# Performance work log

Measured on AMD Instinct MI355X. Metric: run time of the kernel, lower is better.

The kernel has to match this reference:

```python
import jax, jax.numpy as jnp
import numpy as np

D = 768
H = 12
DH = D // H
EPS = 1e-5

def _ln(x, g, b):
    m = jnp.mean(x, axis=-1, keepdims=True)
    v = jnp.mean(jnp.square(x - m), axis=-1, keepdims=True)
    return (x - m) * jax.lax.rsqrt(v + EPS) * g + b

def _gelu_new(x):
    c = jnp.float32(0.7978845608028654)  # sqrt(2/pi)
    return 0.5 * x * (1.0 + jnp.tanh(c * (x + 0.044715 * x * x * x)))

def setup_inputs() -> dict:
    key = jax.random.key(0)
    ks = jax.random.split(key, 12)
    s = lambda fan: 1.0 / np.sqrt(fan)
    return {
        "x": jax.random.normal(ks[0], (2, 1024, D), jnp.float32),
        "context_seq": jax.random.normal(ks[1], (2, 256, D), jnp.float32),
        "sos_h": jnp.zeros((D,), jnp.float32),
        "ln1_g": jnp.ones((D,), jnp.float32),
        "ln1_b": jnp.zeros((D,), jnp.float32),
        "W_attn": jax.random.normal(ks[2], (D, 3 * D), jnp.float32) * s(D),
        "b_attn": jnp.zeros((3 * D,), jnp.float32),
        "W_ref": jax.random.normal(ks[3], (D, 2 * D), jnp.float32) * s(D),
        "b_ref": jnp.zeros((2 * D,), jnp.float32),
        "W_proj": jax.random.normal(ks[4], (D, D), jnp.float32) * s(D),
        "b_proj": jnp.zeros((D,), jnp.float32),
        "ln2_g": jnp.ones((D,), jnp.float32),
        "ln2_b": jnp.zeros((D,), jnp.float32),
        "W_fc": jax.random.normal(ks[5], (D, 4 * D), jnp.float32) * s(D),
        "b_fc": jnp.zeros((4 * D,), jnp.float32),
        "W_mproj": jax.random.normal(ks[6], (4 * D, D), jnp.float32) * s(4 * D),
        "b_mproj": jnp.zeros((D,), jnp.float32),
    }

def _split_heads(t):  # [B,T,D] -> [B,H,T,dh]
    B, T, _ = t.shape
    return t.reshape(B, T, H, DH).transpose(0, 2, 1, 3)

def reference(x, context_seq, sos_h, ln1_g, ln1_b, W_attn, b_attn, W_ref, b_ref,
              W_proj, b_proj, ln2_g, ln2_b, W_fc, b_fc, W_mproj, b_mproj):
    B, S, _ = x.shape
    Sc = context_seq.shape[1]
    # prepend sos token (history_seq is None, history_seq_len = 0)
    sos = jnp.broadcast_to(sos_h.reshape(1, 1, D), (B, 1, D))
    h = jnp.concatenate([sos, x], axis=1)          # [B, S+1, D]
    hl = _ln(h, ln1_g, ln1_b)
    qkv = hl @ W_attn + b_attn
    q, k, v = jnp.split(qkv, 3, axis=-1)
    ckv = context_seq @ W_ref + b_ref
    kc, vc = jnp.split(ckv, 2, axis=-1)
    K = jnp.concatenate([kc, k], axis=1)            # [B, Sc+S+1, D]
    V = jnp.concatenate([vc, v], axis=1)
    qh, kh, vh = _split_heads(q), _split_heads(K), _split_heads(V)
    nd, ns = S + 1, Sc + S + 1
    w = jnp.einsum('bhqd,bhkd->bhqk', qh, kh) / jnp.float32(np.sqrt(DH))
    # causal bias window: query i attends to key j iff j <= i + Sc
    mask = jnp.arange(ns)[None, :] <= (jnp.arange(nd)[:, None] + Sc)
    w = jnp.where(mask[None, None], w, jnp.float32(-10000.0))
    w = jax.nn.softmax(w, axis=-1)
    a = jnp.einsum('bhqk,bhkd->bhqd', w, vh)        # [B,H,S+1,dh]
    a = a.transpose(0, 2, 1, 3).reshape(B, nd, D)
    a = a @ W_proj + b_proj
    h = h + a
    m = _gelu_new(_ln(h, ln2_g, ln2_b) @ W_fc + b_fc) @ W_mproj + b_mproj
    h = h + m
    return h[:, 1:, :]                               # drop sos position
```

## Files before the change

### kernel.cpp

```cpp
#include <hip/hip_runtime.h>
#include <math.h>

#define D0 768
#define NH 12
#define DHD 64
#define NB 2
#define SQ 1024
#define SCX 256
#define ND 1025
#define NS 1281
#define TT (NB*ND)
#define TP 2176
#define TC (NB*SCX)

typedef __attribute__((ext_vector_type(8))) short bf16x8;
typedef __attribute__((ext_vector_type(4))) float f32x4;

typedef const __attribute__((address_space(1))) unsigned int* gptr_t;
typedef __attribute__((address_space(3))) unsigned int* lptr_t;

__device__ __forceinline__ unsigned short f2bf(float f) {
    union { float f; unsigned u; } v; v.f = f;
    unsigned r = v.u + 0x7FFFu + ((v.u >> 16) & 1u);
    return (unsigned short)(r >> 16);
}

__device__ __forceinline__ float gelu_new(float x) {
    float x3 = x*x*x;
    float u = 0.7978845608028654f*(x + 0.044715f*x3);
    return 0.5f*x*(1.f + tanhf(u));
}

struct PrepArgs {
    const float* x; const float* sos; float* h;
    const float* ctx; unsigned short* ctxb;
    const float* W[5]; unsigned short* Wt[5];
    int K[5], N[5], nblk[5];
};

#define NBH 1538
#define NCVT 192

__global__ __launch_bounds__(256) void k_prep(PrepArgs a) {
    __shared__ float t[32][33];
    const int tid = threadIdx.x;
    int bid = blockIdx.x;
    if (bid < NBH) {
        int idx = bid*256 + tid;
        if (idx < TT*192) {
            int r = idx/192, c4 = idx%192;
            int b = r/ND, tt = r%ND;
            float4 v;
            if (tt == 0) v = ((const float4*)a.sos)[c4];
            else         v = ((const float4*)a.x)[(size_t)(b*SQ + tt - 1)*192 + c4];
            ((float4*)a.h)[(size_t)r*192 + c4] = v;
        }
        return;
    }
    bid -= NBH;
    if (bid < NCVT) {
        int i = bid*256 + tid;
        float4 p = ((const float4*)a.ctx)[i*2];
        float4 q = ((const float4*)a.ctx)[i*2+1];
        uint4 o;
        o.x = (unsigned)f2bf(p.x) | ((unsigned)f2bf(p.y) << 16);
        o.y = (unsigned)f2bf(p.z) | ((unsigned)f2bf(p.w) << 16);
        o.z = (unsigned)f2bf(q.x) | ((unsigned)f2bf(q.y) << 16);
        o.w = (unsigned)f2bf(q.z) | ((unsigned)f2bf(q.w) << 16);
        ((uint4*)a.ctxb)[i] = o;
        return;
    }
    bid -= NCVT;
    #pragma unroll
    for (int wi = 0; wi < 5; ++wi) {
        if (bid < a.nblk[wi]) {
            const float* W = a.W[wi];
            unsigned short* Wt = a.Wt[wi];
            const int K = a.K[wi], N = a.N[wi];
            const int nbx = N >> 5;
            const int n0 = (bid % nbx)*32, k0 = (bid / nbx)*32;
            const int r = tid >> 3, c4 = (tid & 7)*4;
            float4 v = *(const float4*)&W[(size_t)(k0+r)*N + n0 + c4];
            t[r][c4+0]=v.x; t[r][c4+1]=v.y; t[r][c4+2]=v.z; t[r][c4+3]=v.w;
            __syncthreads();
            ushort4 o;
            o.x = f2bf(t[c4+0][r]); o.y = f2bf(t[c4+1][r]);
            o.z = f2bf(t[c4+2][r]); o.w = f2bf(t[c4+3][r]);
            *(ushort4*)&Wt[(size_t)(n0+r)*K + k0 + c4] = o;
            return;
        }
        bid -= a.nblk[wi];
    }
}

__global__ __launch_bounds__(256) void k_ln(const float* __restrict__ in,
                                            const float* __restrict__ add,
                                            const float* __restrict__ g,
                                            const float* __restrict__ beta,
                                            unsigned short* __restrict__ out,
                                            float* __restrict__ resid,
                                            int nvalid) {
    int r = blockIdx.x;
    int tid = threadIdx.x;
    const size_t base = (size_t)r*D0;
    if (r >= nvalid) {
        out[base+tid] = 0; out[base+tid+256] = 0; out[base+tid+512] = 0;
        return;
    }
    float v0 = in[base+tid], v1 = in[base+tid+256], v2 = in[base+tid+512];
    if (add) {
        v0 += add[base+tid]; v1 += add[base+tid+256]; v2 += add[base+tid+512];
        resid[base+tid] = v0; resid[base+tid+256] = v1; resid[base+tid+512] = v2;
    }
    float s = v0+v1+v2;
    float ss = v0*v0 + v1*v1 + v2*v2;
    #pragma unroll
    for (int o = 32; o >= 1; o >>= 1) {
        s  += __shfl_down(s, o);
        ss += __shfl_down(ss, o);
    }
    __shared__ float red[8];
    __shared__ float mv[2];
    int w = tid >> 6;
    if ((tid & 63) == 0) { red[w] = s; red[4+w] = ss; }
    __syncthreads();
    if (tid == 0) {
        float S1 = red[0]+red[1]+red[2]+red[3];
        float S2 = red[4]+red[5]+red[6]+red[7];
        float mean = S1 * (1.f/D0);
        float var  = S2 * (1.f/D0) - mean*mean;
        mv[0] = mean; mv[1] = rsqrtf(var + 1e-5f);
    }
    __syncthreads();
    float mean = mv[0], rstd = mv[1];
    out[base+tid]     = f2bf((v0-mean)*rstd*g[tid]     + beta[tid]);
    out[base+tid+256] = f2bf((v1-mean)*rstd*g[tid+256] + beta[tid+256]);
    out[base+tid+512] = f2bf((v2-mean)*rstd*g[tid+512] + beta[tid+512]);
}

template<int GELU, int OUTBF>
__device__ __forceinline__ void gemm64_body(unsigned short* As, unsigned short* Bs,
                                            const unsigned short* __restrict__ A,
                                            const unsigned short* __restrict__ Bt,
                                            const float* __restrict__ bias,
                                            void* __restrict__ Cv,
                                            int N, int K, int bx, int by) {
    const int tid = threadIdx.x;
    const int w = tid >> 6;
    const int l = tid & 63;
    const int wm = w >> 1, wn = w & 1;
    const int m0 = by * 64, n0 = bx * 64;

    f32x4 acc[2][2] = {};

    for (int k0 = 0; k0 < K; k0 += 64) {
        __syncthreads();
        #pragma unroll
        for (int i = 0; i < 2; ++i) {
            int s = i*256 + tid;
            int row = s >> 3;
            int ch  = (s & 7) ^ (row & 7);
            const unsigned short* ga = A  + (size_t)(m0 + row)*K + k0 + ch*8;
            const unsigned short* gb = Bt + (size_t)(n0 + row)*K + k0 + ch*8;
            lptr_t la = (lptr_t)(As + (i*256 + w*64)*8);
            lptr_t lb = (lptr_t)(Bs + (i*256 + w*64)*8);
            __builtin_amdgcn_global_load_lds((gptr_t)ga, la, 16, 0, 0);
            __builtin_amdgcn_global_load_lds((gptr_t)gb, lb, 16, 0, 0);
        }
        __syncthreads();
        #pragma unroll
        for (int kc = 0; kc < 2; ++kc) {
            const int kchunk = kc*4 + (l >> 4);
            bf16x8 a[2], b[2];
            #pragma unroll
            for (int mi = 0; mi < 2; ++mi) {
                int row = wm*32 + mi*16 + (l & 15);
                a[mi] = *(const bf16x8*)&As[row*64 + ((kchunk ^ (row & 7))*8)];
            }
            #pragma unroll
            for (int ni = 0; ni < 2; ++ni) {
                int row = wn*32 + ni*16 + (l & 15);
                b[ni] = *(const bf16x8*)&Bs[row*64 + ((kchunk ^ (row & 7))*8)];
            }
            #pragma unroll
            for (int mi = 0; mi < 2; ++mi)
                #pragma unroll
                for (int ni = 0; ni < 2; ++ni)
                    acc[mi][ni] = __builtin_amdgcn_mfma_f32_16x16x32_bf16(a[mi], b[ni], acc[mi][ni], 0, 0, 0);
        }
    }

    float* Cf = (float*)Cv;
    unsigned short* Cb = (unsigned short*)Cv;
    const int rbase = m0 + wm*32 + (l >> 4)*4;
    const int cbase = n0 + wn*32 + (l & 15);
    #pragma unroll
    for (int ni = 0; ni < 2; ++ni) {
        int col = cbase + ni*16;
        float bv = bias[col];
        #pragma unroll
        for (int mi = 0; mi < 2; ++mi) {
            #pragma unroll
            for (int r = 0; r < 4; ++r) {
                int row = rbase + mi*16 + r;
                float v = acc[mi][ni][r] + bv;
                if (GELU) v = gelu_new(v);
                if (OUTBF) Cb[(size_t)row*N + col] = f2bf(v);
                else       Cf[(size_t)row*N + col] = v;
            }
        }
    }
}

template<int GELU, int OUTBF>
__global__ __launch_bounds__(256) void k_gemm64(const unsigned short* __restrict__ A,
                                                const unsigned short* __restrict__ Bt,
                                                const float* __restrict__ bias,
                                                void* __restrict__ Cv,
                                                int N, int K) {
    __shared__ unsigned short As[64*64];
    __shared__ unsigned short Bs[64*64];
    gemm64_body<GELU,OUTBF>(As, Bs, A, Bt, bias, Cv, N, K, blockIdx.x, blockIdx.y);
}

__global__ __launch_bounds__(256) void k_gemm_qkvckv(const unsigned short* __restrict__ hlb,
                                                     const unsigned short* __restrict__ WatT,
                                                     const float* __restrict__ bat,
                                                     unsigned short* __restrict__ qkvb,
                                                     const unsigned short* __restrict__ ctxb,
                                                     const unsigned short* __restrict__ WrefT,
                                                     const float* __restrict__ bref,
                                                     unsigned short* __restrict__ ckvb) {
    __shared__ unsigned short As[64*64];
    __shared__ unsigned short Bs[64*64];
    int bid = blockIdx.x;
    if (bid < (2304/64)*(TP/64)) {
        gemm64_body<0,1>(As, Bs, hlb, WatT, bat, qkvb, 2304, 768, bid % (2304/64), bid / (2304/64));
    } else {
        bid -= (2304/64)*(TP/64);
        gemm64_body<0,1>(As, Bs, ctxb, WrefT, bref, ckvb, 1536, 768, bid % (1536/64), bid / (1536/64));
    }
}

__global__ __launch_bounds__(256, 4) void k_attn_mfma(const unsigned short* __restrict__ qkvb,
                                                      const unsigned short* __restrict__ ckvb,
                                                      unsigned short* __restrict__ attnob) {
    const int bh = blockIdx.y;
    const int b = bh / NH, hh = bh % NH;
    const int tid = threadIdx.x;
    const int w = tid >> 6;
    const int l = tid & 63;
    const int lg = l >> 4;
    const int ll = l & 15;

    const int q0 = (64 - blockIdx.x) * 16;

    __shared__ unsigned short lds_u16[18432];
    unsigned short* Kw = lds_u16 + w*4608;
    unsigned short* Vw = Kw + 2048;
    unsigned short* Pw = Kw + 4096;

    bf16x8 qf[2];
    {
        int qc = min(q0 + ll, ND-1);
        const unsigned short* qrow = qkvb + (size_t)(b*ND + qc)*2304 + hh*64;
        qf[0] = *(const bf16x8*)(qrow + lg*8);
        qf[1] = *(const bf16x8*)(qrow + 32 + lg*8);
    }

    f32x4 o_acc[4] = {};
    float mrow[4], lrow[4];
    #pragma unroll
    for (int i = 0; i < 4; ++i) { mrow[i] = -1e30f; lrow[i] = 0.f; }

    const int klim = min(q0 + 15 + SCX, NS-1);

    for (int kt = w; kt*32 <= klim; kt += 4) {
        #pragma unroll
        for (int it = 0; it < 4; ++it) {
            int slot = it*64 + l;
            int key  = slot >> 3;
            int ch   = (slot & 7) ^ (key & 7);
            int kg   = min(kt*32 + key, NS-1);
            const unsigned short* src = (kg < SCX)
                ? ckvb + (size_t)(b*SCX + kg)*1536 + hh*64 + ch*8
                : qkvb + (size_t)(b*ND + kg - SCX)*2304 + 768 + hh*64 + ch*8;
            __builtin_amdgcn_global_load_lds((gptr_t)src, (lptr_t)(Kw + it*512), 16, 0, 0);
        }
        #pragma unroll
        for (int it = 0; it < 2; ++it) {
            int kp  = l & 15;
            int dch = (l >> 4) + it*4;
            int kv0 = kp*2;
            int kg0 = min(kt*32 + kv0,     NS-1);
            int kg1 = min(kt*32 + kv0 + 1, NS-1);
            const unsigned short* s0 = (kg0 < SCX)
                ? ckvb + (size_t)(b*SCX + kg0)*1536 + 768 + hh*64 + dch*8
                : qkvb + (size_t)(b*ND + kg0 - SCX)*2304 + 1536 + hh*64 + dch*8;
            const unsigned short* s1 = (kg1 < SCX)
                ? ckvb + (size_t)(b*SCX + kg1)*1536 + 768 + hh*64 + dch*8
                : qkvb + (size_t)(b*ND + kg1 - SCX)*2304 + 1536 + hh*64 + dch*8;
            union { uint4 u; unsigned short s[8]; } r0, r1;
            r0.u = *(const uint4*)s0;
            r1.u = *(const uint4*)s1;
            #pragma unroll
            for (int j = 0; j < 8; ++j) {
                int d = dch*8 + j;
                unsigned val = (unsigned)r0.s[j] | ((unsigned)r1.s[j] << 16);
                *(unsigned*)(Vw + d*32 + (((kp>>2) ^ ((d>>2)&3))*8) + (kp&3)*2) = val;
            }
        }
        asm volatile("s_waitcnt vmcnt(0) lgkmcnt(0)" ::: "memory");
        __builtin_amdgcn_sched_barrier(0);

        bf16x8 kf[2][2];
        #pragma unroll
        for (int c = 0; c < 2; ++c) {
            int key = c*16 + ll;
            #pragma unroll
            for (int kc = 0; kc < 2; ++kc)
                kf[c][kc] = *(const bf16x8*)(Kw + key*64 + (((kc*4 + lg) ^ (key&7))*8));
        }
        f32x4 s_acc[2];
        #pragma unroll
        for (int c = 0; c < 2; ++c) {
            f32x4 z = {0.f, 0.f, 0.f, 0.f};
            z = __builtin_amdgcn_mfma_f32_16x16x32_bf16(qf[0], kf[c][0], z, 0, 0, 0);
            s_acc[c] = __builtin_amdgcn_mfma_f32_16x16x32_bf16(qf[1], kf[c][1], z, 0, 0, 0);
        }

        const int kbase = kt*32;
        if (kbase + 31 > q0 + SCX) {
            #pragma unroll
            for (int c = 0; c < 2; ++c) {
                int key = kbase + c*16 + ll;
                #pragma unroll
                for (int i = 0; i < 4; ++i) {
                    int q = q0 + lg*4 + i;
                    if (key > q + SCX) s_acc[c][i] = -1e30f;
                }
            }
        }

        float tmax[4];
        #pragma unroll
        for (int i = 0; i < 4; ++i) {
            float tm = fmaxf(s_acc[0][i], s_acc[1][i]);
            #pragma unroll
            for (int o = 1; o < 16; o <<= 1) tm = fmaxf(tm, __shfl_xor(tm, o));
            tmax[i] = tm;
        }
        #pragma unroll
        for (int i = 0; i < 4; ++i) {
            float mnew = fmaxf(mrow[i], tmax[i]*0.125f);
            float fs = __expf(mrow[i] - mnew);
            mrow[i] = mnew;
            lrow[i] *= fs;
            #pragma unroll
            for (int dc = 0; dc < 4; ++dc) o_acc[dc][i] *= fs;
        }
        float psum[4] = {0.f, 0.f, 0.f, 0.f};
        #pragma unroll
        for (int c = 0; c < 2; ++c) {
            int kv = c*16 + ll;
            #pragma unroll
            for (int i = 0; i < 4; ++i) {
                float p = __expf(fmaf(s_acc[c][i], 0.125f, -mrow[i]));
                psum[i] += p;
                int q = lg*4 + i;
                union { float f; unsigned u; } cv; cv.f = p;
                Pw[q*32 + (((kv>>3) ^ ((q>>2)&3))*8) + (kv&7)]
                    = (unsigned short)((cv.u + 0x8000u) >> 16);
            }
        }
        #pragma unroll
        for (int i = 0; i < 4; ++i) {
            float s = psum[i];
            #pragma unroll
            for (int o = 1; o < 16; o <<= 1) s += __shfl_xor(s, o);
            lrow[i] += s;
        }

        bf16x8 pf = *(const bf16x8*)(Pw + ll*32 + ((lg ^ ((ll>>2)&3))*8));
        #pragma unroll
        for (int dc = 0; dc < 4; ++dc) {
            int d = dc*16 + ll;
            bf16x8 vf = *(const bf16x8*)(Vw + d*32 + ((lg ^ ((d>>2)&3))*8));
            o_acc[dc] = __builtin_amdgcn_mfma_f32_16x16x32_bf16(pf, vf, o_acc[dc], 0, 0, 0);
        }
    }

    __syncthreads();
    {
        float* Om = (float*)(lds_u16 + w*2176);
        float* ml = (float*)(lds_u16 + 8704 + w*64);
        #pragma unroll
        for (int dc = 0; dc < 4; ++dc)
            #pragma unroll
            for (int i = 0; i < 4; ++i)
                Om[(lg*4 + i)*68 + dc*16 + ll] = o_acc[dc][i];
        if (ll == 0) {
            #pragma unroll
            for (int i = 0; i < 4; ++i) {
                ml[(lg*4 + i)*2]     = mrow[i];
                ml[(lg*4 + i)*2 + 1] = lrow[i];
            }
        }
    }
    __syncthreads();
    #pragma unroll
    for (int i = 0; i < 4; ++i) {
        int row = lg*4 + i;
        float mw[4], lw[4];
        #pragma unroll
        for (int wp = 0; wp < 4; ++wp) {
            const float* mlp = (const float*)(lds_u16 + 8704 + wp*64);
            mw[wp] = mlp[row*2]; lw[wp] = mlp[row*2 + 1];
        }
        float M = fmaxf(fmaxf(mw[0], mw[1]), fmaxf(mw[2], mw[3]));
        float L = 0.f, acc = 0.f;
        #pragma unroll
        for (int wp = 0; wp < 4; ++wp) {
            float sc = __expf(mw[wp] - M);
            L += lw[wp]*sc;
            acc += sc * ((const float*)(lds_u16 + wp*2176))[row*68 + w*16 + ll];
        }
        int q = q0 + row;
        if (q < ND)
            attnob[(size_t)(b*ND + q)*768 + hh*64 + w*16 + ll] = f2bf(acc / L);
    }
}

__global__ void k_final(const float* __restrict__ h, const float* __restrict__ mp,
                        float* __restrict__ out) {
    int idx = blockIdx.x*blockDim.x + threadIdx.x;
    const int total = NB*SQ*192;
    if (idx >= total) return;
    int r = idx/192, c4 = idx%192;
    int b = r/SQ, t = r%SQ;
    size_t hr = (size_t)(b*ND + t + 1)*192 + c4;
    float4 hv = ((const float4*)h)[hr];
    float4 mv = ((const float4*)mp)[hr];
    ((float4*)out)[idx] = make_float4(hv.x+mv.x, hv.y+mv.y, hv.z+mv.z, hv.w+mv.w);
}

extern "C" void kernel_launch(void* const* d_in, const int* in_sizes, int n_in,
                              void* d_out, int out_size, void* d_ws, size_t ws_size,
                              hipStream_t stream) {
    const float* x     = (const float*)d_in[0];
    const float* ctx   = (const float*)d_in[1];
    const float* sos   = (const float*)d_in[2];
    const float* ln1g  = (const float*)d_in[3];
    const float* ln1b  = (const float*)d_in[4];
    const float* Wat   = (const float*)d_in[5];
    const float* bat   = (const float*)d_in[6];
    const float* Wref  = (const float*)d_in[7];
    const float* bref  = (const float*)d_in[8];
    const float* Wpj   = (const float*)d_in[9];
    const float* bpj   = (const float*)d_in[10];
    const float* ln2g  = (const float*)d_in[11];
    const float* ln2b  = (const float*)d_in[12];
    const float* Wfc   = (const float*)d_in[13];
    const float* bfc   = (const float*)d_in[14];
    const float* Wmp   = (const float*)d_in[15];
    const float* bmp   = (const float*)d_in[16];
    float* out = (float*)d_out;

    char* p = (char*)d_ws;
    float* h      = (float*)p;  p += (size_t)TP*768*4;
    float* aproj  = (float*)p;  p += (size_t)TP*768*4;
    unsigned short* qkvb   = (unsigned short*)p;  p += (size_t)TP*2304*2;
    unsigned short* ckvb   = (unsigned short*)p;  p += (size_t)TC*1536*2;
    unsigned short* hlb    = (unsigned short*)p;  p += (size_t)TP*768*2;
    unsigned short* attnob = (unsigned short*)p;  p += (size_t)TP*768*2;
    unsigned short* mfcb   = (unsigned short*)p;  p += (size_t)TP*3072*2;
    unsigned short* ctxb   = (unsigned short*)p;  p += (size_t)TC*768*2;
    unsigned short* WatT   = (unsigned short*)p;  p += (size_t)2304*768*2;
    unsigned short* WrefT  = (unsigned short*)p;  p += (size_t)1536*768*2;
    unsigned short* WpjT   = (unsigned short*)p;  p += (size_t)768*768*2;
    unsigned short* WfcT   = (unsigned short*)p;  p += (size_t)3072*768*2;
    unsigned short* WmpT   = (unsigned short*)p;  p += (size_t)768*3072*2;

    PrepArgs pa;
    pa.x = x; pa.sos = sos; pa.h = h; pa.ctx = ctx; pa.ctxb = ctxb;
    pa.W[0]=Wat;  pa.Wt[0]=WatT;  pa.K[0]=768;  pa.N[0]=2304; pa.nblk[0]=(2304/32)*(768/32);
    pa.W[1]=Wref; pa.Wt[1]=WrefT; pa.K[1]=768;  pa.N[1]=1536; pa.nblk[1]=(1536/32)*(768/32);
    pa.W[2]=Wpj;  pa.Wt[2]=WpjT;  pa.K[2]=768;  pa.N[2]=768;  pa.nblk[2]=(768/32)*(768/32);
    pa.W[3]=Wfc;  pa.Wt[3]=WfcT;  pa.K[3]=768;  pa.N[3]=3072; pa.nblk[3]=(3072/32)*(768/32);
    pa.W[4]=Wmp;  pa.Wt[4]=WmpT;  pa.K[4]=3072; pa.N[4]=768;  pa.nblk[4]=(768/32)*(3072/32);
    int nprep = NBH + NCVT + pa.nblk[0]+pa.nblk[1]+pa.nblk[2]+pa.nblk[3]+pa.nblk[4];

    k_prep<<<dim3(nprep), dim3(256), 0, stream>>>(pa);
    k_ln<<<dim3(TP), dim3(256), 0, stream>>>(h, nullptr, ln1g, ln1b, hlb, nullptr, TT);
    k_gemm_qkvckv<<<dim3((2304/64)*(TP/64) + (1536/64)*(TC/64)), dim3(256), 0, stream>>>(
        hlb, WatT, bat, qkvb, ctxb, WrefT, bref, ckvb);
    k_attn_mfma<<<dim3(65, NB*NH), dim3(256), 0, stream>>>(qkvb, ckvb, attnob);
    k_gemm64<0,0><<<dim3(768/64, TP/64), dim3(256), 0, stream>>>(attnob, WpjT, bpj, aproj, 768, 768);
    k_ln<<<dim3(TP), dim3(256), 0, stream>>>(h, aproj, ln2g, ln2b, hlb, h, TT);
    k_gemm64<1,1><<<dim3(3072/64, TP/64), dim3(256), 0, stream>>>(hlb, WfcT, bfc, mfcb, 3072, 768);
    k_gemm64<0,0><<<dim3(768/64, TP/64), dim3(256), 0, stream>>>(mfcb, WmpT, bmp, aproj, 768, 3072);
    k_final<<<dim3((NB*SQ*192 + 255)/256), dim3(256), 0, stream>>>(h, aproj, out);
}
```

Measured before the change: 263.6 us.

## Pre-pack K and transposed V per head, load fragments directly from global

A new kernel copies K into a contiguous per-head buffer and writes V transposed per head, padded to 1344 keys. Attention then loads MFMA fragments straight from these buffers instead of staging K and V through LDS each tile. Each block now covers 32 queries, with two waves per 16-query group splitting the key tiles, so the final merge combines two partial softmax states instead of four. This removes the per-tile LDS staging, transposition and waitcnt stalls. It costs an extra launch plus global traffic for the repacked K/V, and the fragment loads rely on cache hits.

```diff
diff --git a/kernel.cpp b/kernel.cpp
--- a/kernel.cpp
+++ b/kernel.cpp
@@ -12,6 +12,7 @@
 #define TT (NB*ND)
 #define TP 2176
 #define TC (NB*SCX)
+#define KP 1344
 
 typedef __attribute__((ext_vector_type(8))) short bf16x8;
 typedef __attribute__((ext_vector_type(4))) float f32x4;
@@ -242,8 +243,40 @@
     }
 }
 
+__global__ __launch_bounds__(256) void k_kvt(const unsigned short* __restrict__ qkvb,
+                                             const unsigned short* __restrict__ ckvb,
+                                             unsigned short* __restrict__ kU,
+                                             unsigned short* __restrict__ vT) {
+    const int bh = blockIdx.y;
+    const int b = bh / NH, hh = bh % NH;
+    const int key0 = blockIdx.x * 32;
+    const int tid = threadIdx.x;
+    __shared__ unsigned short tv[64][34];
+    const int r = tid >> 3, c = tid & 7;
+    const int kg = key0 + r;
+    uint4 kvv = make_uint4(0,0,0,0), vvv = make_uint4(0,0,0,0);
+    if (kg < NS) {
+        const unsigned short* src = (kg < SCX)
+            ? ckvb + (size_t)(b*SCX + kg)*1536 + hh*64 + c*8
+            : qkvb + (size_t)(b*ND + kg - SCX)*2304 + 768 + hh*64 + c*8;
+        kvv = *(const uint4*)src;
+        vvv = *(const uint4*)(src + 768);
+    }
+    *(uint4*)(kU + ((size_t)bh*KP + key0 + r)*64 + c*8) = kvv;
+    union { uint4 u; unsigned short s[8]; } vu; vu.u = vvv;
+    #pragma unroll
+    for (int j = 0; j < 8; ++j) tv[c*8 + j][r] = vu.s[j];
+    __syncthreads();
+    const int d = tid >> 2, kc = tid & 3;
+    unsigned short o[8];
+    #pragma unroll
+    for (int j = 0; j < 8; ++j) o[j] = tv[d][kc*8 + j];
+    *(uint4*)(vT + ((size_t)bh*64 + d)*KP + key0 + kc*8) = *(uint4*)o;
+}
+
 __global__ __launch_bounds__(256, 4) void k_attn_mfma(const unsigned short* __restrict__ qkvb,
-                                                      const unsigned short* __restrict__ ckvb,
+                                                      const unsigned short* __restrict__ kU,
+                                                      const unsigned short* __restrict__ vT,
                                                       unsigned short* __restrict__ attnob) {
     const int bh = blockIdx.y;
     const int b = bh / NH, hh = bh % NH;
@@ -252,13 +285,17 @@
     const int l = tid & 63;
     const int lg = l >> 4;
     const int ll = l & 15;
-
-    const int q0 = (64 - blockIdx.x) * 16;
-
-    __shared__ unsigned short lds_u16[18432];
-    unsigned short* Kw = lds_u16 + w*4608;
-    unsigned short* Vw = Kw + 2048;
-    unsigned short* Pw = Kw + 4096;
+    const int kvh = w & 1;
+
+    const int q0 = (32 - blockIdx.x)*32 + (w >> 1)*16;
+
+    __shared__ unsigned short Ps[4][512];
+    __shared__ float Om[4][16][68];
+    __shared__ float Ml[4][16][2];
+
+    const unsigned short* kB = kU + (size_t)bh*KP*64;
+    const unsigned short* vB = vT + (size_t)bh*64*KP;
+    unsigned short* Pw = Ps[w];
 
     bf16x8 qf[2];
     {
@@ -273,54 +310,22 @@
     #pragma unroll
     for (int i = 0; i < 4; ++i) { mrow[i] = -1e30f; lrow[i] = 0.f; }
 
-    const int klim = min(q0 + 15 + SCX, NS-1);
-
-    for (int kt = w; kt*32 <= klim; kt += 4) {
-        #pragma unroll
-        for (int it = 0; it < 4; ++it) {
-            int slot = it*64 + l;
-            int key  = slot >> 3;
-            int ch   = (slot & 7) ^ (key & 7);
-            int kg   = min(kt*32 + key, NS-1);
-            const unsigned short* src = (kg < SCX)
-                ? ckvb + (size_t)(b*SCX + kg)*1536 + hh*64 + ch*8
-                : qkvb + (size_t)(b*ND + kg - SCX)*2304 + 768 + hh*64 + ch*8;
-            __builtin_amdgcn_global_load_lds((gptr_t)src, (lptr_t)(Kw + it*512), 16, 0, 0);
-        }
-        #pragma unroll
-        for (int it = 0; it < 2; ++it) {
-            int kp  = l & 15;
-            int dch = (l >> 4) + it*4;
-            int kv0 = kp*2;
-            int kg0 = min(kt*32 + kv0,     NS-1);
-            int kg1 = min(kt*32 + kv0 + 1, NS-1);
-            const unsigned short* s0 = (kg0 < SCX)
-                ? ckvb + (size_t)(b*SCX + kg0)*1536 + 768 + hh*64 + dch*8
-                : qkvb + (size_t)(b*ND + kg0 - SCX)*2304 + 1536 + hh*64 + dch*8;
-            const unsigned short* s1 = (kg1 < SCX)
-                ? ckvb + (size_t)(b*SCX + kg1)*1536 + 768 + hh*64 + dch*8
-                : qkvb + (size_t)(b*ND + kg1 - SCX)*2304 + 1536 + hh*64 + dch*8;
-            union { uint4 u; unsigned short s[8]; } r0, r1;
-            r0.u = *(const uint4*)s0;
-            r1.u = *(const uint4*)s1;
-            #pragma unroll
-            for (int j = 0; j < 8; ++j) {
-                int d = dch*8 + j;
-                unsigned val = (unsigned)r0.s[j] | ((unsigned)r1.s[j] << 16);
-                *(unsigned*)(Vw + d*32 + (((kp>>2) ^ ((d>>2)&3))*8) + (kp&3)*2) = val;
-            }
-        }
-        asm volatile("s_waitcnt vmcnt(0) lgkmcnt(0)" ::: "memory");
-        __builtin_amdgcn_sched_barrier(0);
-
+    const int nt = (q0 + 15 + SCX)/32 + 1;
+
+    for (int kt = kvh; kt < nt; kt += 2) {
+        const int kbase = kt*32;
         bf16x8 kf[2][2];
         #pragma unroll
         for (int c = 0; c < 2; ++c) {
-            int key = c*16 + ll;
-            #pragma unroll
-            for (int kc = 0; kc < 2; ++kc)
-                kf[c][kc] = *(const bf16x8*)(Kw + key*64 + (((kc*4 + lg) ^ (key&7))*8));
-        }
+            const unsigned short* krow = kB + (size_t)(kbase + c*16 + ll)*64;
+            kf[c][0] = *(const bf16x8*)(krow + lg*8);
+            kf[c][1] = *(const bf16x8*)(krow + 32 + lg*8);
+        }
+        bf16x8 vf[4];
+        #pragma unroll
+        for (int dc = 0; dc < 4; ++dc)
+            vf[dc] = *(const bf16x8*)(vB + (size_t)(dc*16 + ll)*KP + kbase + lg*8);
+
         f32x4 s_acc[2];
         #pragma unroll
         for (int c = 0; c < 2; ++c) {
@@ -329,7 +334,6 @@
             s_acc[c] = __builtin_amdgcn_mfma_f32_16x16x32_bf16(qf[1], kf[c][1], z, 0, 0, 0);
         }
 
-        const int kbase = kt*32;
         if (kbase + 31 > q0 + SCX) {
             #pragma unroll
             for (int c = 0; c < 2; ++c) {
@@ -383,51 +387,43 @@
 
         bf16x8 pf = *(const bf16x8*)(Pw + ll*32 + ((lg ^ ((ll>>2)&3))*8));
         #pragma unroll
-        for (int dc = 0; dc < 4; ++dc) {
-            int d = dc*16 + ll;
-            bf16x8 vf = *(const bf16x8*)(Vw + d*32 + ((lg ^ ((d>>2)&3))*8));
-            o_acc[dc] = __builtin_amdgcn_mfma_f32_16x16x32_bf16(pf, vf, o_acc[dc], 0, 0, 0);
-        }
+        for (int dc = 0; dc < 4; ++dc)
+            o_acc[dc] = __builtin_amdgcn_mfma_f32_16x16x32_bf16(pf, vf[dc], o_acc[dc], 0, 0, 0);
     }
 
     __syncthreads();
-    {
-        float* Om = (float*)(lds_u16 + w*2176);
-        float* ml = (float*)(lds_u16 + 8704 + w*64);
-        #pragma unroll
-        for (int dc = 0; dc < 4; ++dc)
-            #pragma unroll
-            for (int i = 0; i < 4; ++i)
-                Om[(lg*4 + i)*68 + dc*16 + ll] = o_acc[dc][i];
-        if (ll == 0) {
-            #pragma unroll
-            for (int i = 0; i < 4; ++i) {
-                ml[(lg*4 + i)*2]     = mrow[i];
-                ml[(lg*4 + i)*2 + 1] = lrow[i];
-            }
+    #pragma unroll
+    for (int dc = 0; dc < 4; ++dc)
+        #pragma unroll
+        for (int i = 0; i < 4; ++i)
+            Om[w][lg*4 + i][dc*16 + ll] = o_acc[dc][i];
+    if (ll == 0) {
+        #pragma unroll
+        for (int i = 0; i < 4; ++i) {
+            Ml[w][lg*4 + i][0] = mrow[i];
+            Ml[w][lg*4 + i][1] = lrow[i];
         }
     }
     __syncthreads();
+    const int pw = w ^ 1;
     #pragma unroll
     for (int i = 0; i < 4; ++i) {
         int row = lg*4 + i;
-        float mw[4], lw[4];
-        #pragma unroll
-        for (int wp = 0; wp < 4; ++wp) {
-            const float* mlp = (const float*)(lds_u16 + 8704 + wp*64);
-            mw[wp] = mlp[row*2]; lw[wp] = mlp[row*2 + 1];
-        }
-        float M = fmaxf(fmaxf(mw[0], mw[1]), fmaxf(mw[2], mw[3]));
-        float L = 0.f, acc = 0.f;
-        #pragma unroll
-        for (int wp = 0; wp < 4; ++wp) {
-            float sc = __expf(mw[wp] - M);
-            L += lw[wp]*sc;
-            acc += sc * ((const float*)(lds_u16 + wp*2176))[row*68 + w*16 + ll];
-        }
+        float m0 = Ml[w][row][0],  l0 = Ml[w][row][1];
+        float m1 = Ml[pw][row][0], l1 = Ml[pw][row][1];
+        float M  = fmaxf(m0, m1);
+        float e0 = __expf(m0 - M), e1 = __expf(m1 - M);
+        float L  = l0*e0 + l1*e1;
         int q = q0 + row;
-        if (q < ND)
-            attnob[(size_t)(b*ND + q)*768 + hh*64 + w*16 + ll] = f2bf(acc / L);
+        if (q < ND) {
+            unsigned short* orow = attnob + (size_t)(b*ND + q)*768 + hh*64;
+            #pragma unroll
+            for (int dc2 = 0; dc2 < 2; ++dc2) {
+                int d = kvh*32 + dc2*16 + ll;
+                float acc = e0*Om[w][row][d] + e1*Om[pw][row][d];
+                orow[d] = f2bf(acc / L);
+            }
+        }
     }
 }
 
@@ -475,6 +471,8 @@
     unsigned short* attnob = (unsigned short*)p;  p += (size_t)TP*768*2;
     unsigned short* mfcb   = (unsigned short*)p;  p += (size_t)TP*3072*2;
     unsigned short* ctxb   = (unsigned short*)p;  p += (size_t)TC*768*2;
+    unsigned short* kU     = (unsigned short*)p;  p += (size_t)NB*NH*KP*64*2;
+    unsigned short* vT     = (unsigned short*)p;  p += (size_t)NB*NH*KP*64*2;
     unsigned short* WatT   = (unsigned short*)p;  p += (size_t)2304*768*2;
     unsigned short* WrefT  = (unsigned short*)p;  p += (size_t)1536*768*2;
     unsigned short* WpjT   = (unsigned short*)p;  p += (size_t)768*768*2;
@@ -494,7 +492,8 @@
     k_ln<<<dim3(TP), dim3(256), 0, stream>>>(h, nullptr, ln1g, ln1b, hlb, nullptr, TT);
     k_gemm_qkvckv<<<dim3((2304/64)*(TP/64) + (1536/64)*(TC/64)), dim3(256), 0, stream>>>(
         hlb, WatT, bat, qkvb, ctxb, WrefT, bref, ckvb);
-    k_attn_mfma<<<dim3(65, NB*NH), dim3(256), 0, stream>>>(qkvb, ckvb, attnob);
+    k_kvt<<<dim3(KP/32, NB*NH), dim3(256), 0, stream>>>(qkvb, ckvb, kU, vT);
+    k_attn_mfma<<<dim3(33, NB*NH), dim3(256), 0, stream>>>(qkvb, kU, vT, attnob);
     k_gemm64<0,0><<<dim3(768/64, TP/64), dim3(256), 0, stream>>>(attnob, WpjT, bpj, aproj, 768, 768);
     k_ln<<<dim3(TP), dim3(256), 0, stream>>>(h, aproj, ln2g, ln2b, hlb, h, TT);
     k_gemm64<1,1><<<dim3(3072/64, TP/64), dim3(256), 0, stream>>>(hlb, WfcT, bfc, mfcb, 3072, 768);
```

New measurement: 271.1 us. +2.9%, slower.
